# Kernel tuning notes

Measured on AMD Instinct MI355X. Metric: run time of the kernel, lower is better.

## Reference

```python
import jax, jax.numpy as jnp
import numpy as np

N = 2048          # target nodes
N_NODES = 2048    # neighbor pool
D_IN = 256
D_EDGE = 16
D_HID = 32
D_OUT = 256


def _mlp(h, w1, b1, w2, b2):
    # Linear -> Tanh -> Linear
    return jnp.tanh(h @ w1 + b1) @ w2 + b2


def setup_inputs() -> dict:
    key = jax.random.key(0)
    ks = jax.random.split(key, 20)
    s = 0.05
    inp = {
        "x": jax.random.normal(ks[0], (N, D_IN), jnp.float32),
        "neibs": jax.random.normal(ks[1], (N_NODES, D_IN), jnp.float32),
        "edge_emb": jax.random.normal(ks[2], (N * N_NODES, D_EDGE), jnp.float32),
        # multiplicative binary mask (float, as in original ws * mask)
        "mask": (jax.random.uniform(ks[3], (N, N_NODES)) < 0.7).astype(jnp.float32),
        "ax_w1": jax.random.normal(ks[4], (D_IN, D_HID), jnp.float32) * s,
        "ax_b1": jnp.zeros((D_HID,), jnp.float32),
        "ax_w2": jax.random.normal(ks[5], (D_HID, D_HID), jnp.float32) * s,
        "ax_b2": jnp.zeros((D_HID,), jnp.float32),
        "an_w1": jax.random.normal(ks[6], (D_IN, D_HID), jnp.float32) * s,
        "an_b1": jnp.zeros((D_HID,), jnp.float32),
        "an_w2": jax.random.normal(ks[7], (D_HID, D_HID), jnp.float32) * s,
        "an_b2": jnp.zeros((D_HID,), jnp.float32),
        "ae_w1": jax.random.normal(ks[8], (D_EDGE, D_HID), jnp.float32) * s,
        "ae_b1": jnp.zeros((D_HID,), jnp.float32),
        "ae_w2": jax.random.normal(ks[9], (D_HID, D_HID), jnp.float32) * s,
        "ae_b2": jnp.zeros((D_HID,), jnp.float32),
        "fcx_w": jax.random.normal(ks[10], (2 * D_IN, D_OUT), jnp.float32) * s,
        "fcx_b": jnp.zeros((D_OUT,), jnp.float32),
    }
    return inp


def reference(x, neibs, edge_emb, mask,
              ax_w1, ax_b1, ax_w2, ax_b2,
              an_w1, an_b1, an_w2, an_b2,
              ae_w1, ae_b1, ae_w2, ae_b2,
              fcx_w, fcx_b):
    x_att = _mlp(x, ax_w1, ax_b1, ax_w2, ax_b2)          # (N, H)
    neib_att = _mlp(neibs, an_w1, an_b1, an_w2, an_b2)   # (n_nodes, H)
    # edge attention is computed in the original forward but never used (dead code)
    _edge_att = _mlp(edge_emb, ae_w1, ae_b1, ae_w2, ae_b2)
    # multiplicative masking (NOT additive -inf), then softmax over neighbors
    ws = jnp.einsum('nh,mh->nm', x_att, neib_att) * mask  # (N, n_nodes)
    ws = jax.nn.softmax(ws, axis=1)
    agg_neib = jax.nn.sigmoid(ws @ neibs)                 # (N, D_IN)
    # concat_node=False path: concat -> fc_x -> sigmoid; dropout is identity (eval)
    out = jax.nn.sigmoid(jnp.concatenate([x, agg_neib], axis=1) @ fcx_w + fcx_b)
    return out
```

## Files before the change

kernel.cpp:

```cpp
#include <hip/hip_runtime.h>
#include <hip/hip_bf16.h>
#include <math.h>

#define NROWS 2048
#define DIN 256
#define DH 32
#define DOUT 256

typedef unsigned short ushort_t;
typedef unsigned int uint_t;
typedef __attribute__((ext_vector_type(8))) short short8;
typedef __attribute__((ext_vector_type(4))) float floatx4;

__device__ __forceinline__ float bf2f(uint_t u) {
    union { uint_t i; float f; } v; v.i = u << 16; return v.f;
}
__device__ __forceinline__ ushort_t f2bf(float f) {
    __hip_bfloat16 h = __float2bfloat16(f);
    union { __hip_bfloat16 h; ushort_t u; } v; v.h = h; return v.u;
}
__device__ __forceinline__ float sigm(float v) { return 1.0f / (1.0f + __expf(-v)); }

#define PSTR 2056
#define ASTR 520

__global__ __launch_bounds__(256) void prep_kernel(
    const float* __restrict__ x, const float* __restrict__ neibs,
    const float* __restrict__ ax_w1, const float* __restrict__ ax_b1,
    const float* __restrict__ ax_w2, const float* __restrict__ ax_b2,
    const float* __restrict__ an_w1, const float* __restrict__ an_b1,
    const float* __restrict__ an_w2, const float* __restrict__ an_b2,
    const float* __restrict__ fcx_w,
    ushort_t* __restrict__ x_attB, short8* __restrict__ n_attP,
    short8* __restrict__ B_pack, short8* __restrict__ W_pack)
{
    __shared__ float smem[32 * 256];
    const int t = threadIdx.x;
    const int b = blockIdx.x;

    if (b < 512) {
        float (*srow)[DIN] = (float (*)[DIN])smem;
        float* hbuf = smem + 8 * DIN;
        float* sbuf = smem + 8 * DIN + 8 * DH;

        const bool is_x = b < 256;
        const int row0 = (is_x ? b : b - 256) * 8;
        const float* __restrict__ in = is_x ? x : neibs;
        const float* __restrict__ w1 = is_x ? ax_w1 : an_w1;
        const float* __restrict__ b1 = is_x ? ax_b1 : an_b1;
        const float* __restrict__ w2 = is_x ? ax_w2 : an_w2;
        const float* __restrict__ b2 = is_x ? ax_b2 : an_b2;

        const int r = t >> 5, c = t & 31;
        {
            const float4* in4 = (const float4*)(in + (size_t)(row0 + r) * DIN);
            float4 a = in4[c * 2], bb = in4[c * 2 + 1];
            *(float4*)&srow[r][c * 8] = a;
            *(float4*)&srow[r][c * 8 + 4] = bb;
        }
        __syncthreads();

        float s = b1[c];
#pragma unroll 8
        for (int k = 0; k < DIN; ++k) s += srow[r][k] * w1[k * DH + c];
        s = tanhf(s);
        hbuf[r * DH + c] = s;
        __syncthreads();

        float s2 = b2[c];
#pragma unroll
        for (int j = 0; j < DH; ++j) s2 += hbuf[r * DH + j] * w2[j * DH + c];

        if (is_x) {
            x_attB[(size_t)(row0 + r) * DH + c] = f2bf(s2);
        } else {
            sbuf[r * DH + c] = s2;
            __syncthreads();
            if (t < 32) {
                const int r2 = t >> 2, q = t & 3;
                const int row = row0 + r2;
                short8 v;
#pragma unroll
                for (int j = 0; j < 8; ++j) v[j] = (short)f2bf(sbuf[r2 * DH + q * 8 + j]);
                n_attP[(row >> 4) * 64 + q * 16 + (row & 15)] = v;
            }
        }
    } else if (b < 576) {
        const int s = b - 512;
        float* tile = smem;
#pragma unroll
        for (int i = 0; i < 8; ++i) {
            const int e = i * 256 + t;
            const int row = e >> 6, c4 = e & 63;
            const float4 v = ((const float4*)neibs)[(size_t)(32 * s + row) * 64 + c4];
            *(float4*)&tile[row * 256 + c4 * 4] = v;
        }
        __syncthreads();
#pragma unroll
        for (int i = 0; i < 4; ++i) {
            const int G = i * 256 + t;
            const int n = G & 15, q = (G >> 4) & 3, tt = (G >> 6) & 3, w = G >> 8;
            const int col = w * 64 + tt * 16 + n;
            short8 v;
#pragma unroll
            for (int j = 0; j < 8; ++j) v[j] = (short)f2bf(tile[(8 * q + j) * 256 + col]);
            B_pack[s * 1024 + G] = v;
        }
    } else {
        const int s = b - 576;
        float* tile = smem;
#pragma unroll
        for (int i = 0; i < 8; ++i) {
            const int e = i * 256 + t;
            const int row = e >> 6, c4 = e & 63;
            const float4 v = ((const float4*)fcx_w)[(size_t)(32 * s + row) * 64 + c4];
            *(float4*)&tile[row * 256 + c4 * 4] = v;
        }
        __syncthreads();
#pragma unroll
        for (int i = 0; i < 4; ++i) {
            const int G = i * 256 + t;
            const int n = G & 15, q = (G >> 4) & 3, tt = (G >> 6) & 3, w = G >> 8;
            const int col = w * 64 + tt * 16 + n;
            short8 v;
#pragma unroll
            for (int j = 0; j < 8; ++j) v[j] = (short)f2bf(tile[(8 * q + j) * 256 + col]);
            W_pack[s * 1024 + G] = v;
        }
    }
}

__global__ __launch_bounds__(512, 2) void attn_kernel(
    const float* __restrict__ x, const float* __restrict__ mask,
    const ushort_t* __restrict__ x_attB, const short8* __restrict__ n_attP,
    const short8* __restrict__ B_pack, const short8* __restrict__ W_pack,
    const float* __restrict__ fcx_b, float* __restrict__ out)
{
    __shared__ __align__(16) ushort_t pTr[8 * PSTR];
    __shared__ __align__(16) ushort_t ATr[8 * ASTR];
    __shared__ float row_inv[8];

    const int t = threadIdx.x;
    const int n0 = blockIdx.x * 8;
    const int w = t >> 6, lane = t & 63;
    const int q = lane >> 4, nn = lane & 15;
    const int arow = lane & 7;
    const int rbase = (lane >> 4) * 4;

#pragma unroll
    for (int i = 0; i < 4; ++i) {
        const int e = i * 512 + t;
        const int r = e >> 8, k = e & 255;
        ATr[r * ASTR + k] = f2bf(x[(size_t)(n0 + r) * DIN + k]);
    }

    const short8 av_s = *(const short8*)(x_attB + (size_t)(n0 + arow) * DH + q * 8);
#pragma unroll 4
    for (int i = 0; i < 16; ++i) {
        const int tl = w * 16 + i;
        const short8 bv = n_attP[tl * 64 + lane];
        floatx4 c = __builtin_amdgcn_mfma_f32_16x16x32_bf16(
            av_s, bv, (floatx4){0.f, 0.f, 0.f, 0.f}, 0, 0, 0);
        if (lane < 32) {
            const int m = tl * 16 + nn;
#pragma unroll
            for (int rg = 0; rg < 4; ++rg) {
                const int row = rbase + rg;
                const float sv = c[rg] * mask[(size_t)(n0 + row) * NROWS + m];
                pTr[row * PSTR + m] = f2bf(sv);
            }
        }
    }
    __syncthreads();

    {
        ushort_t* prow = pTr + w * PSTR;
        uint_t raw[16];
        float mx = -1e30f;
#pragma unroll
        for (int j = 0; j < 16; ++j) {
            raw[j] = *(const uint_t*)(prow + j * 128 + 2 * lane);
            mx = fmaxf(mx, fmaxf(bf2f(raw[j] & 0xffffu), bf2f(raw[j] >> 16)));
        }
#pragma unroll
        for (int off = 32; off >= 1; off >>= 1) mx = fmaxf(mx, __shfl_xor(mx, off));
        float sum = 0.f;
#pragma unroll
        for (int j = 0; j < 16; ++j) {
            const float e0 = __expf(bf2f(raw[j] & 0xffffu) - mx);
            const float e1 = __expf(bf2f(raw[j] >> 16) - mx);
            sum += e0 + e1;
            *(uint_t*)(prow + j * 128 + 2 * lane) =
                (uint_t)f2bf(e0) | ((uint_t)f2bf(e1) << 16);
        }
#pragma unroll
        for (int off = 32; off >= 1; off >>= 1) sum += __shfl_xor(sum, off);
        if (lane == 0) row_inv[w] = 1.f / sum;
    }
    __syncthreads();

    const int cq = w & 3, kh = w >> 2;
    const char* aBase = (const char*)pTr + arow * (PSTR * 2);
    floatx4 acc[4];
#pragma unroll
    for (int tt = 0; tt < 4; ++tt) acc[tt] = (floatx4){0.f, 0.f, 0.f, 0.f};

#pragma unroll 4
    for (int si = 0; si < 32; ++si) {
        const int s = kh * 32 + si;
        const short8 av = *(const short8*)(aBase + s * 64 + q * 16);
#pragma unroll
        for (int tt = 0; tt < 4; ++tt) {
            const short8 bv = B_pack[(s * 16 + cq * 4 + tt) * 64 + lane];
            acc[tt] = __builtin_amdgcn_mfma_f32_16x16x32_bf16(av, bv, acc[tt], 0, 0, 0);
        }
    }
    __syncthreads();
    float* red = (float*)pTr;
    if (kh == 1) {
#pragma unroll
        for (int tt = 0; tt < 4; ++tt)
            *(floatx4*)&red[((cq * 4 + tt) * 64 + lane) * 4] = acc[tt];
    }
    __syncthreads();
    if (kh == 0) {
#pragma unroll
        for (int tt = 0; tt < 4; ++tt) {
            const floatx4 rv = *(const floatx4*)&red[((cq * 4 + tt) * 64 + lane) * 4];
            acc[tt] += rv;
        }
        if (lane < 32) {
#pragma unroll
            for (int tt = 0; tt < 4; ++tt) {
                const int n = cq * 64 + tt * 16 + nn;
#pragma unroll
                for (int rg = 0; rg < 4; ++rg) {
                    const int row = rbase + rg;
                    ATr[row * ASTR + 256 + n] = f2bf(sigm(acc[tt][rg] * row_inv[row]));
                }
            }
        }
    }
    __syncthreads();

    const char* a2 = (const char*)ATr + arow * (ASTR * 2);
    floatx4 acc2[4];
#pragma unroll
    for (int tt = 0; tt < 4; ++tt) acc2[tt] = (floatx4){0.f, 0.f, 0.f, 0.f};

#pragma unroll
    for (int si = 0; si < 8; ++si) {
        const int s = kh * 8 + si;
        const short8 av = *(const short8*)(a2 + s * 64 + q * 16);
#pragma unroll
        for (int tt = 0; tt < 4; ++tt) {
            const short8 bv = W_pack[(s * 16 + cq * 4 + tt) * 64 + lane];
            acc2[tt] = __builtin_amdgcn_mfma_f32_16x16x32_bf16(av, bv, acc2[tt], 0, 0, 0);
        }
    }
    __syncthreads();
    if (kh == 1) {
#pragma unroll
        for (int tt = 0; tt < 4; ++tt)
            *(floatx4*)&red[((cq * 4 + tt) * 64 + lane) * 4] = acc2[tt];
    }
    __syncthreads();
    if (kh == 0) {
#pragma unroll
        for (int tt = 0; tt < 4; ++tt) {
            const floatx4 rv = *(const floatx4*)&red[((cq * 4 + tt) * 64 + lane) * 4];
            acc2[tt] += rv;
        }
        if (lane < 32) {
#pragma unroll
            for (int tt = 0; tt < 4; ++tt) {
                const int n = cq * 64 + tt * 16 + nn;
                const float bias = fcx_b[n];
#pragma unroll
                for (int rg = 0; rg < 4; ++rg) {
                    const int row = rbase + rg;
                    out[(size_t)(n0 + row) * DOUT + n] = sigm(acc2[tt][rg] + bias);
                }
            }
        }
    }
}

extern "C" void kernel_launch(void* const* d_in, const int* in_sizes, int n_in,
                              void* d_out, int out_size, void* d_ws, size_t ws_size,
                              hipStream_t stream) {
    const float* x      = (const float*)d_in[0];
    const float* neibs  = (const float*)d_in[1];
    const float* mask   = (const float*)d_in[3];
    const float* ax_w1  = (const float*)d_in[4];
    const float* ax_b1  = (const float*)d_in[5];
    const float* ax_w2  = (const float*)d_in[6];
    const float* ax_b2  = (const float*)d_in[7];
    const float* an_w1  = (const float*)d_in[8];
    const float* an_b1  = (const float*)d_in[9];
    const float* an_w2  = (const float*)d_in[10];
    const float* an_b2  = (const float*)d_in[11];
    const float* fcx_w  = (const float*)d_in[16];
    const float* fcx_b  = (const float*)d_in[17];
    float* out = (float*)d_out;

    char* ws = (char*)d_ws;
    ushort_t* x_attB = (ushort_t*)ws;
    short8*   n_attP = (short8*)(ws + 131072);
    short8*   B_pack = (short8*)(ws + 262144);
    short8*   W_pack = (short8*)(ws + 1310720);

    prep_kernel<<<592, 256, 0, stream>>>(
        x, neibs, ax_w1, ax_b1, ax_w2, ax_b2,
        an_w1, an_b1, an_w2, an_b2, fcx_w,
        x_attB, n_attP, B_pack, W_pack);

    attn_kernel<<<256, 512, 0, stream>>>(
        x, mask, x_attB, n_attP, B_pack, W_pack, fcx_b, out);
}
```

Before: 384.9 us.

## Split GEMM output columns across all waves, removing cross-wave K reduction

The two MFMA GEMMs now give each of the 8 waves its own 32 output columns over the full K range, instead of splitting K in half and reducing through shared memory. This drops two barriers and LDS round trips per GEMM and lets every lane store results, using the MFMA's duplicated rows. Two accumulator sets alternate per K step to break dependency chains. The packed B and W layouts are remapped to match, and the x staging now uses float4 loads.

```diff
diff --git a/kernel.cpp b/kernel.cpp
--- a/kernel.cpp
+++ b/kernel.cpp
@@ -11,6 +11,7 @@
 typedef unsigned int uint_t;
 typedef __attribute__((ext_vector_type(8))) short short8;
 typedef __attribute__((ext_vector_type(4))) float floatx4;
+typedef __attribute__((ext_vector_type(4))) ushort_t ushortx4;
 
 __device__ __forceinline__ float bf2f(uint_t u) {
     union { uint_t i; float f; } v; v.i = u << 16; return v.f;
@@ -99,8 +100,8 @@
 #pragma unroll
         for (int i = 0; i < 4; ++i) {
             const int G = i * 256 + t;
-            const int n = G & 15, q = (G >> 4) & 3, tt = (G >> 6) & 3, w = G >> 8;
-            const int col = w * 64 + tt * 16 + n;
+            const int n = G & 15, q = (G >> 4) & 3, ct = G >> 6;
+            const int col = ct * 16 + n;
             short8 v;
 #pragma unroll
             for (int j = 0; j < 8; ++j) v[j] = (short)f2bf(tile[(8 * q + j) * 256 + col]);
@@ -120,8 +121,8 @@
 #pragma unroll
         for (int i = 0; i < 4; ++i) {
             const int G = i * 256 + t;
-            const int n = G & 15, q = (G >> 4) & 3, tt = (G >> 6) & 3, w = G >> 8;
-            const int col = w * 64 + tt * 16 + n;
+            const int n = G & 15, q = (G >> 4) & 3, ct = G >> 6;
+            const int col = ct * 16 + n;
             short8 v;
 #pragma unroll
             for (int j = 0; j < 8; ++j) v[j] = (short)f2bf(tile[(8 * q + j) * 256 + col]);
@@ -145,13 +146,16 @@
     const int w = t >> 6, lane = t & 63;
     const int q = lane >> 4, nn = lane & 15;
     const int arow = lane & 7;
-    const int rbase = (lane >> 4) * 4;
-
-#pragma unroll
-    for (int i = 0; i < 4; ++i) {
-        const int e = i * 512 + t;
-        const int r = e >> 8, k = e & 255;
-        ATr[r * ASTR + k] = f2bf(x[(size_t)(n0 + r) * DIN + k]);
+    const int gl = lane >> 4;
+    const int prow0 = (gl & 1) * 4 + (gl >> 1) * 2;
+    const int reg0 = (gl >> 1) * 2;
+
+    {
+        const int r = t >> 6, c4 = t & 63;
+        const float4 v = *(const float4*)(x + (size_t)(n0 + r) * DIN + c4 * 4);
+        ushortx4 o;
+        o.x = f2bf(v.x); o.y = f2bf(v.y); o.z = f2bf(v.z); o.w = f2bf(v.w);
+        *(ushortx4*)&ATr[r * ASTR + c4 * 4] = o;
     }
 
     const short8 av_s = *(const short8*)(x_attB + (size_t)(n0 + arow) * DH + q * 8);
@@ -161,14 +165,12 @@
         const short8 bv = n_attP[tl * 64 + lane];
         floatx4 c = __builtin_amdgcn_mfma_f32_16x16x32_bf16(
             av_s, bv, (floatx4){0.f, 0.f, 0.f, 0.f}, 0, 0, 0);
-        if (lane < 32) {
-            const int m = tl * 16 + nn;
-#pragma unroll
-            for (int rg = 0; rg < 4; ++rg) {
-                const int row = rbase + rg;
-                const float sv = c[rg] * mask[(size_t)(n0 + row) * NROWS + m];
-                pTr[row * PSTR + m] = f2bf(sv);
-            }
+        const int m = tl * 16 + nn;
+#pragma unroll
+        for (int u = 0; u < 2; ++u) {
+            const int row = prow0 + u;
+            const float sv = c[reg0 + u] * mask[(size_t)(n0 + row) * NROWS + m];
+            pTr[row * PSTR + m] = f2bf(sv);
         }
     }
     __syncthreads();
@@ -199,89 +201,61 @@
     }
     __syncthreads();
 
-    const int cq = w & 3, kh = w >> 2;
     const char* aBase = (const char*)pTr + arow * (PSTR * 2);
-    floatx4 acc[4];
-#pragma unroll
-    for (int tt = 0; tt < 4; ++tt) acc[tt] = (floatx4){0.f, 0.f, 0.f, 0.f};
+    floatx4 accP[2][2];
+#pragma unroll
+    for (int tt = 0; tt < 2; ++tt)
+#pragma unroll
+        for (int pr = 0; pr < 2; ++pr) accP[tt][pr] = (floatx4){0.f, 0.f, 0.f, 0.f};
 
 #pragma unroll 4
-    for (int si = 0; si < 32; ++si) {
-        const int s = kh * 32 + si;
+    for (int s = 0; s < 64; ++s) {
         const short8 av = *(const short8*)(aBase + s * 64 + q * 16);
-#pragma unroll
-        for (int tt = 0; tt < 4; ++tt) {
-            const short8 bv = B_pack[(s * 16 + cq * 4 + tt) * 64 + lane];
-            acc[tt] = __builtin_amdgcn_mfma_f32_16x16x32_bf16(av, bv, acc[tt], 0, 0, 0);
+        const int pr = s & 1;
+#pragma unroll
+        for (int tt = 0; tt < 2; ++tt) {
+            const short8 bv = B_pack[(s * 16 + 2 * w + tt) * 64 + lane];
+            accP[tt][pr] = __builtin_amdgcn_mfma_f32_16x16x32_bf16(av, bv, accP[tt][pr], 0, 0, 0);
+        }
+    }
+#pragma unroll
+    for (int tt = 0; tt < 2; ++tt) {
+        const floatx4 a = accP[tt][0] + accP[tt][1];
+        const int n = w * 32 + tt * 16 + nn;
+#pragma unroll
+        for (int u = 0; u < 2; ++u) {
+            const int row = prow0 + u;
+            ATr[row * ASTR + 256 + n] = f2bf(sigm(a[reg0 + u] * row_inv[row]));
         }
     }
     __syncthreads();
-    float* red = (float*)pTr;
-    if (kh == 1) {
-#pragma unroll
-        for (int tt = 0; tt < 4; ++tt)
-            *(floatx4*)&red[((cq * 4 + tt) * 64 + lane) * 4] = acc[tt];
-    }
-    __syncthreads();
-    if (kh == 0) {
-#pragma unroll
-        for (int tt = 0; tt < 4; ++tt) {
-            const floatx4 rv = *(const floatx4*)&red[((cq * 4 + tt) * 64 + lane) * 4];
-            acc[tt] += rv;
-        }
-        if (lane < 32) {
-#pragma unroll
-            for (int tt = 0; tt < 4; ++tt) {
-                const int n = cq * 64 + tt * 16 + nn;
-#pragma unroll
-                for (int rg = 0; rg < 4; ++rg) {
-                    const int row = rbase + rg;
-                    ATr[row * ASTR + 256 + n] = f2bf(sigm(acc[tt][rg] * row_inv[row]));
-                }
-            }
-        }
-    }
-    __syncthreads();
 
     const char* a2 = (const char*)ATr + arow * (ASTR * 2);
-    floatx4 acc2[4];
-#pragma unroll
-    for (int tt = 0; tt < 4; ++tt) acc2[tt] = (floatx4){0.f, 0.f, 0.f, 0.f};
-
-#pragma unroll
-    for (int si = 0; si < 8; ++si) {
-        const int s = kh * 8 + si;
+    floatx4 acc2[2][2];
+#pragma unroll
+    for (int tt = 0; tt < 2; ++tt)
+#pragma unroll
+        for (int pr = 0; pr < 2; ++pr) acc2[tt][pr] = (floatx4){0.f, 0.f, 0.f, 0.f};
+
+#pragma unroll
+    for (int s = 0; s < 16; ++s) {
         const short8 av = *(const short8*)(a2 + s * 64 + q * 16);
-#pragma unroll
-        for (int tt = 0; tt < 4; ++tt) {
-            const short8 bv = W_pack[(s * 16 + cq * 4 + tt) * 64 + lane];
-            acc2[tt] = __builtin_amdgcn_mfma_f32_16x16x32_bf16(av, bv, acc2[tt], 0, 0, 0);
-        }
-    }
-    __syncthreads();
-    if (kh == 1) {
-#pragma unroll
-        for (int tt = 0; tt < 4; ++tt)
-            *(floatx4*)&red[((cq * 4 + tt) * 64 + lane) * 4] = acc2[tt];
-    }
-    __syncthreads();
-    if (kh == 0) {
-#pragma unroll
-        for (int tt = 0; tt < 4; ++tt) {
-            const floatx4 rv = *(const floatx4*)&red[((cq * 4 + tt) * 64 + lane) * 4];
-            acc2[tt] += rv;
-        }
-        if (lane < 32) {
-#pragma unroll
-            for (int tt = 0; tt < 4; ++tt) {
-                const int n = cq * 64 + tt * 16 + nn;
-                const float bias = fcx_b[n];
-#pragma unroll
-                for (int rg = 0; rg < 4; ++rg) {
-                    const int row = rbase + rg;
-                    out[(size_t)(n0 + row) * DOUT + n] = sigm(acc2[tt][rg] + bias);
-                }
-            }
+        const int pr = s & 1;
+#pragma unroll
+        for (int tt = 0; tt < 2; ++tt) {
+            const short8 bv = W_pack[(s * 16 + 2 * w + tt) * 64 + lane];
+            acc2[tt][pr] = __builtin_amdgcn_mfma_f32_16x16x32_bf16(av, bv, acc2[tt][pr], 0, 0, 0);
+        }
+    }
+#pragma unroll
+    for (int tt = 0; tt < 2; ++tt) {
+        const floatx4 a = acc2[tt][0] + acc2[tt][1];
+        const int n = w * 32 + tt * 16 + nn;
+        const float bias = fcx_b[n];
+#pragma unroll
+        for (int u = 0; u < 2; ++u) {
+            const int row = prow0 + u;
+            out[(size_t)(n0 + row) * DOUT + n] = sigm(a[reg0 + u] + bias);
         }
     }
 }
```

New measurement: 373.6 us. 1.03x faster.
